# Performance work log

Measured on AMD Instinct MI355X. Metric: run time of the kernel, lower is better.

The kernel has to match this reference:

```python
import jax, jax.numpy as jnp
import numpy as np

TEMPERATURE = 0.1

def setup_inputs() -> dict:
    key = jax.random.key(0)
    k1, k2 = jax.random.split(key)
    A = jax.random.normal(k1, (16, 2048, 256), dtype=jnp.float32)
    B = jax.random.normal(k2, (16, 2048, 256), dtype=jnp.float32)
    return {"A": A, "B": B}

def _l2norm(x):
    # F.normalize(p=2, dim=-1): x / max(||x||, eps), eps=1e-12
    n = jnp.sqrt(jnp.sum(x * x, axis=-1, keepdims=True))
    return x / jnp.maximum(n, 1e-12)

def _nce_dir(sim):
    # sim: (B, N, N) logits; labels are the diagonal (row n -> col n)
    # mean over all B*N rows of (logsumexp(row) - row[label])
    lse = jax.nn.logsumexp(sim, axis=-1)            # (B, N)
    diag = jnp.diagonal(sim, axis1=-2, axis2=-1)    # (B, N)
    return jnp.mean(lse - diag)

def reference(A, B):
    emb1 = _l2norm(A)
    emb2 = _l2norm(B)
    sim12 = jnp.einsum("bnc,bmc->bnm", emb1, emb2) / TEMPERATURE  # (B, N, N)
    # sim21 is sim12 transposed per batch; reuse instead of a second bmm
    sim21 = jnp.swapaxes(sim12, -1, -2)
    return _nce_dir(sim12) + _nce_dir(sim21)
```

## Files before the change

### kernel.cpp

```cpp
#include <hip/hip_runtime.h>
#include <hip/hip_bf16.h>

typedef __attribute__((ext_vector_type(8))) __bf16 bf16x8;
typedef __attribute__((ext_vector_type(16))) float f32x16;

#define SCALE_L2E 14.4269504088896f
#define NTOT 32768

#define AS_GLOBAL __attribute__((address_space(1)))
#define AS_LDS    __attribute__((address_space(3)))

__device__ inline void async_copy16(const void* g, void* l) {
    __builtin_amdgcn_global_load_lds((const AS_GLOBAL void*)g, (AS_LDS void*)l, 16, 0, 0);
}

__device__ inline unsigned int f2bf(float f) {
    unsigned int u = __builtin_bit_cast(unsigned int, f);
    u += 0x7fffu + ((u >> 16) & 1u);
    return u >> 16;
}

__device__ inline uint4 pack8(float4 x, float4 y, float s) {
    uint4 r;
    r.x = f2bf(x.x * s) | (f2bf(x.y * s) << 16);
    r.y = f2bf(x.z * s) | (f2bf(x.w * s) << 16);
    r.z = f2bf(y.x * s) | (f2bf(y.y * s) << 16);
    r.w = f2bf(y.z * s) | (f2bf(y.w * s) << 16);
    return r;
}

__device__ inline float dot8(float4 x, float4 y) {
    return x.x*y.x + x.y*y.y + x.z*y.z + x.w*y.w;
}

__global__ __launch_bounds__(256) void nrm_kernel(
        const float* __restrict__ A, const float* __restrict__ B,
        uint4* __restrict__ E1f, uint4* __restrict__ E2f,
        float* __restrict__ diagPart, float* __restrict__ scalars,
        unsigned int* __restrict__ counter) {
    __shared__ uint4 E1lds[1024];
    __shared__ uint4 E2lds[1024];
    __shared__ float part[4];

    const int tid = threadIdx.x, w = tid >> 6, l = tid & 63;
    const int q = l & 31, h = l >> 5;
    const int wid = blockIdx.x * 4 + w;

    const float4* A4 = (const float4*)A + ((size_t)wid * 8 + h) * 64 + q * 2;
    const float4* B4 = (const float4*)B + ((size_t)wid * 8 + h) * 64 + q * 2;

    float4 a[8], bb[8];
    #pragma unroll
    for (int i = 0; i < 4; ++i) {
        a[2*i]    = A4[i * 128];
        a[2*i+1]  = A4[i * 128 + 1];
        bb[2*i]   = B4[i * 128];
        bb[2*i+1] = B4[i * 128 + 1];
    }

    float ddAcc = 0.f;
    #pragma unroll
    for (int i = 0; i < 4; ++i) {
        float sa = dot8(a[2*i], a[2*i]) + dot8(a[2*i+1], a[2*i+1]);
        float sb = dot8(bb[2*i], bb[2*i]) + dot8(bb[2*i+1], bb[2*i+1]);
        float dd = dot8(a[2*i], bb[2*i]) + dot8(a[2*i+1], bb[2*i+1]);
        #pragma unroll
        for (int off = 1; off <= 16; off <<= 1) {
            sa += __shfl_xor(sa, off);
            sb += __shfl_xor(sb, off);
            dd += __shfl_xor(dd, off);
        }
        const float ia = 1.0f / fmaxf(sqrtf(sa), 1e-12f);
        const float ib = 1.0f / fmaxf(sqrtf(sb), 1e-12f);
        if (q == 0) ddAcc += dd * ia * ib * 10.0f;

        const int row32 = w * 8 + i * 2 + h;
        const int idx   = (q >> 1) * 64 + (q & 1) * 32 + row32;
        const int idxs  = idx ^ ((idx >> 5) & 7);
        E1lds[idxs] = pack8(a[2*i], a[2*i+1], ia * SCALE_L2E);
        E2lds[idxs] = pack8(bb[2*i], bb[2*i+1], ib);
    }

    #pragma unroll
    for (int off = 1; off <= 32; off <<= 1) ddAcc += __shfl_xor(ddAcc, off);
    if (l == 0) part[w] = ddAcc;
    __syncthreads();

    {
        uint4* g1 = E1f + (size_t)blockIdx.x * 1024;
        uint4* g2 = E2f + (size_t)blockIdx.x * 1024;
        #pragma unroll
        for (int j = 0; j < 4; ++j) {
            const int t = j * 256 + tid;
            const int ts = t ^ ((t >> 5) & 7);
            g1[t] = E1lds[ts];
            g2[t] = E2lds[ts];
        }
    }

    if (tid == 0) diagPart[blockIdx.x] = part[0] + part[1] + part[2] + part[3];
    if (blockIdx.x == 0 && tid == 0) { scalars[0] = 0.f; *counter = 0u; }
}

__global__ __launch_bounds__(256, 2) void gemm_kernel(
        const bf16x8* __restrict__ E1f, const uint4* __restrict__ E2f,
        float* __restrict__ colPart, float* __restrict__ rowPart) {
    __shared__ bf16x8 Bbuf[2][2048];
    __shared__ float colLDS[2048];

    const int tid = threadIdx.x, w = tid >> 6, l = tid & 63;
    const int b = blockIdx.x & 15;
    const int ct = (blockIdx.x >> 4) & 3, rt = blockIdx.x >> 6;

    for (int i = l; i < 512; i += 64) colLDS[w * 512 + i] = 0.f;

    const uint4* Bb = E2f + (size_t)b * 65536 + (size_t)ct * 16384 + l;

    auto stage = [&](int buf, int sg) {
        const uint4* src = Bb + (size_t)sg * 2048 + (w * 8) * 64;
        #pragma unroll
        for (int j = 0; j < 8; ++j)
            async_copy16(src + j * 64, &Bbuf[buf][(w * 8 + j) * 64]);
    };

    stage(0, 0);

    const bf16x8* Af0 = E1f + (size_t)b * 65536 + (size_t)(rt * 8 + w * 2) * 1024 + l;
    const bf16x8* Af1 = Af0 + 1024;
    bf16x8 af0[16], af1[16];
    #pragma unroll
    for (int kt = 0; kt < 16; ++kt) { af0[kt] = Af0[kt * 64]; af1[kt] = Af1[kt * 64]; }

    float rowAcc0[16], rowAcc1[16];
    #pragma unroll
    for (int r = 0; r < 16; ++r) { rowAcc0[r] = 0.f; rowAcc1[r] = 0.f; }

    auto mmpair = [&](f32x16& x0, f32x16& x1, const bf16x8* Bf) {
        #pragma unroll
        for (int r = 0; r < 16; ++r) { x0[r] = 0.f; x1[r] = 0.f; }
        __builtin_amdgcn_s_setprio(1);
        #pragma unroll
        for (int kt = 0; kt < 16; ++kt) {
            bf16x8 bfrag = Bf[kt * 64];
            x0 = __builtin_amdgcn_mfma_f32_32x32x16_bf16(af0[kt], bfrag, x0, 0, 0, 0);
            x1 = __builtin_amdgcn_mfma_f32_32x32x16_bf16(af1[kt], bfrag, x1, 0, 0, 0);
        }
        __builtin_amdgcn_s_setprio(0);
    };

    auto epi = [&](const f32x16& c, float (&rAcc)[16], int slot) {
        float p = 0.f;
        #pragma unroll
        for (int r = 0; r < 16; ++r) {
            float e = __builtin_amdgcn_exp2f(c[r]);
            rAcc[r] += e;
            p += e;
        }
        p += __shfl_xor(p, 32);
        if (l < 32) colLDS[w * 512 + slot * 32 + l] += p;
    };

    f32x16 c0, c1, d0, d1;
    #pragma unroll
    for (int r = 0; r < 16; ++r) d1[r] = -__builtin_inff();

    __syncthreads();

    for (int sg = 0; sg < 8; ++sg) {
        if (sg < 7) stage((sg + 1) & 1, sg + 1);
        const bf16x8* Bf = Bbuf[sg & 1] + l;

        mmpair(c0, c1, Bf);
        epi(d1, rowAcc1, (sg * 2 - 1) & 15);
        epi(c0, rowAcc0, sg * 2);

        mmpair(d0, d1, Bf + 1024);
        epi(c1, rowAcc1, sg * 2);
        epi(d0, rowAcc0, sg * 2 + 1);

        __syncthreads();
    }
    epi(d1, rowAcc1, 15);

    #pragma unroll
    for (int r = 0; r < 16; ++r) {
        #pragma unroll
        for (int off = 1; off <= 16; off <<= 1) {
            rowAcc0[r] += __shfl_xor(rowAcc0[r], off);
            rowAcc1[r] += __shfl_xor(rowAcc1[r], off);
        }
    }
    if ((l & 31) == 0) {
        float* rs = rowPart + (size_t)(b * 4 + ct) * 2048 + rt * 256 + w * 64 + 4 * (l >> 5);
        #pragma unroll
        for (int r = 0; r < 16; ++r) {
            const int rl = (r & 3) + 8 * (r >> 2);
            rs[rl]      = rowAcc0[r];
            rs[rl + 32] = rowAcc1[r];
        }
    }

    __syncthreads();
    float* gcol = colPart + (size_t)((b * 4 + ct) * 8 + rt) * 512;
    for (int i = tid; i < 512; i += 256)
        gcol[i] = colLDS[i] + colLDS[512 + i] + colLDS[1024 + i] + colLDS[1536 + i];
}

__global__ __launch_bounds__(256) void fin_kernel(
        const float* __restrict__ colPart, const float* __restrict__ rowPart,
        const float* __restrict__ diagPart, float* __restrict__ scalars,
        unsigned int* __restrict__ counter, float* __restrict__ out) {
    const int tid = threadIdx.x;
    float s = 0.f;
    #pragma unroll
    for (int k = 0; k < 2; ++k) {
        const int g = blockIdx.x * 512 + k * 256 + tid;
        const float* cp = colPart + (size_t)(((g >> 11) * 4 + ((g >> 9) & 3)) * 8) * 512 + (g & 511);
        float cs = 0.f;
        #pragma unroll
        for (int rt = 0; rt < 8; ++rt) cs += cp[rt * 512];
        const float* rp = rowPart + (size_t)(g >> 11) * 4 * 2048 + (g & 2047);
        float rsum = rp[0] + rp[2048] + rp[4096] + rp[6144];
        s += logf(cs) + logf(rsum);
    }
    #pragma unroll
    for (int off = 1; off <= 32; off <<= 1) s += __shfl_xor(s, off);
    __shared__ float part[4];
    __shared__ unsigned int lastFlag;
    if ((tid & 63) == 0) part[tid >> 6] = s;
    __syncthreads();
    if (tid == 0) {
        atomicAdd(&scalars[0], part[0] + part[1] + part[2] + part[3]);
        __threadfence();
        lastFlag = (atomicAdd(counter, 1u) == 63u) ? 1u : 0u;
    }
    __syncthreads();
    if (lastFlag) {
        float d = diagPart[tid] + diagPart[tid + 256]
                + diagPart[tid + 512] + diagPart[tid + 768];
        #pragma unroll
        for (int off = 1; off <= 32; off <<= 1) d += __shfl_xor(d, off);
        if ((tid & 63) == 0) part[tid >> 6] = d;
        __syncthreads();
        if (tid == 0) {
            const float diag = part[0] + part[1] + part[2] + part[3];
            const float logSum = atomicAdd(&scalars[0], 0.f);
            out[0] = (logSum - 2.0f * diag) / (float)NTOT;
        }
    }
}

extern "C" void kernel_launch(void* const* d_in, const int* in_sizes, int n_in,
                              void* d_out, int out_size, void* d_ws, size_t ws_size,
                              hipStream_t stream) {
    const float* A = (const float*)d_in[0];
    const float* B = (const float*)d_in[1];

    char* w = (char*)d_ws;
    uint4* E1f = (uint4*)w;
    uint4* E2f = (uint4*)(w + (size_t)16 * 1024 * 1024);
    float* colPart = (float*)(w + (size_t)32 * 1024 * 1024);
    float* rowPart = colPart + 262144;
    float* diagPart = rowPart + 131072;
    float* scalars = diagPart + 1024;
    unsigned int* counter = (unsigned int*)(scalars + 1);

    hipLaunchKernelGGL(nrm_kernel, dim3(1024), dim3(256), 0, stream,
                       A, B, E1f, E2f, diagPart, scalars, counter);
    hipLaunchKernelGGL(gemm_kernel, dim3(512), dim3(256), 0, stream,
                       (const bf16x8*)E1f, (const uint4*)E2f, colPart, rowPart);
    hipLaunchKernelGGL(fin_kernel, dim3(64), dim3(256), 0, stream,
                       colPart, rowPart, diagPart, scalars, counter, (float*)d_out);
}
```

Measured before the change: 140.0 us.

## Fuse final log-sum reduction into GEMM kernel via last-block counters

Removes the separate finalize kernel launch. The GEMM blocks now count completions per row group and per column group with atomic counters. The last block to finish a group computes the logs and adds them to a global scalar, and a second counter picks the block that writes the final output. This saves one kernel launch and its serial tail, at the cost of extra atomics and fences in every GEMM block.

Measured after the change: 183.3 us. 30.9% more time.

```diff
diff --git a/kernel.cpp b/kernel.cpp
--- a/kernel.cpp
+++ b/kernel.cpp
@@ -12,6 +12,10 @@
 
 __device__ inline void async_copy16(const void* g, void* l) {
     __builtin_amdgcn_global_load_lds((const AS_GLOBAL void*)g, (AS_LDS void*)l, 16, 0, 0);
+}
+
+__device__ inline float aload(const float* p) {
+    return __hip_atomic_load(p, __ATOMIC_RELAXED, __HIP_MEMORY_SCOPE_AGENT);
 }
 
 __device__ inline unsigned int f2bf(float f) {
@@ -37,7 +41,7 @@
         const float* __restrict__ A, const float* __restrict__ B,
         uint4* __restrict__ E1f, uint4* __restrict__ E2f,
         float* __restrict__ diagPart, float* __restrict__ scalars,
-        unsigned int* __restrict__ counter) {
+        unsigned int* __restrict__ cnts) {
     __shared__ uint4 E1lds[1024];
     __shared__ uint4 E2lds[1024];
     __shared__ float part[4];
@@ -99,18 +103,29 @@
     }
 
     if (tid == 0) diagPart[blockIdx.x] = part[0] + part[1] + part[2] + part[3];
-    if (blockIdx.x == 0 && tid == 0) { scalars[0] = 0.f; *counter = 0u; }
+    if (blockIdx.x == 0) {
+        if (tid == 0) scalars[0] = 0.f;
+        if (tid < 193) cnts[tid] = 0u;
+    }
 }
 
 __global__ __launch_bounds__(256, 2) void gemm_kernel(
         const bf16x8* __restrict__ E1f, const uint4* __restrict__ E2f,
-        float* __restrict__ colPart, float* __restrict__ rowPart) {
+        float* __restrict__ colPart, float* __restrict__ rowPart,
+        const float* __restrict__ diagPart, float* __restrict__ scalars,
+        unsigned int* __restrict__ cnts, float* __restrict__ out) {
     __shared__ bf16x8 Bbuf[2][2048];
     __shared__ float colLDS[2048];
+    __shared__ float redbuf[4];
+    __shared__ unsigned int rrS, rcS, isLastS;
 
     const int tid = threadIdx.x, w = tid >> 6, l = tid & 63;
     const int b = blockIdx.x & 15;
     const int ct = (blockIdx.x >> 4) & 3, rt = blockIdx.x >> 6;
+
+    unsigned int* cntRow = cnts;
+    unsigned int* cntCol = cnts + 128;
+    unsigned int* cnt2   = cnts + 192;
 
     for (int i = l; i < 512; i += 64) colLDS[w * 512 + i] = 0.f;
 
@@ -204,47 +219,66 @@
     float* gcol = colPart + (size_t)((b * 4 + ct) * 8 + rt) * 512;
     for (int i = tid; i < 512; i += 256)
         gcol[i] = colLDS[i] + colLDS[512 + i] + colLDS[1024 + i] + colLDS[1536 + i];
-}
-
-__global__ __launch_bounds__(256) void fin_kernel(
-        const float* __restrict__ colPart, const float* __restrict__ rowPart,
-        const float* __restrict__ diagPart, float* __restrict__ scalars,
-        unsigned int* __restrict__ counter, float* __restrict__ out) {
-    const int tid = threadIdx.x;
-    float s = 0.f;
-    #pragma unroll
-    for (int k = 0; k < 2; ++k) {
-        const int g = blockIdx.x * 512 + k * 256 + tid;
-        const float* cp = colPart + (size_t)(((g >> 11) * 4 + ((g >> 9) & 3)) * 8) * 512 + (g & 511);
-        float cs = 0.f;
-        #pragma unroll
-        for (int rt = 0; rt < 8; ++rt) cs += cp[rt * 512];
-        const float* rp = rowPart + (size_t)(g >> 11) * 4 * 2048 + (g & 2047);
-        float rsum = rp[0] + rp[2048] + rp[4096] + rp[6144];
-        s += logf(cs) + logf(rsum);
-    }
-    #pragma unroll
-    for (int off = 1; off <= 32; off <<= 1) s += __shfl_xor(s, off);
-    __shared__ float part[4];
-    __shared__ unsigned int lastFlag;
-    if ((tid & 63) == 0) part[tid >> 6] = s;
+
+    __threadfence();
     __syncthreads();
     if (tid == 0) {
-        atomicAdd(&scalars[0], part[0] + part[1] + part[2] + part[3]);
-        __threadfence();
-        lastFlag = (atomicAdd(counter, 1u) == 63u) ? 1u : 0u;
-    }
-    __syncthreads();
-    if (lastFlag) {
+        isLastS = 0u;
+        rrS = atomicAdd(&cntRow[b * 8 + rt], 1u);
+        rcS = atomicAdd(&cntCol[b * 4 + ct], 1u);
+    }
+    __syncthreads();
+    const bool doRow = (rrS == 3u), doCol = (rcS == 7u);
+    if (doRow || doCol) __threadfence();
+
+    auto blockSum = [&](float v) {
+        #pragma unroll
+        for (int off = 1; off <= 32; off <<= 1) v += __shfl_xor(v, off);
+        if (l == 0) redbuf[w] = v;
+        __syncthreads();
+        float t = redbuf[0] + redbuf[1] + redbuf[2] + redbuf[3];
+        __syncthreads();
+        return t;
+    };
+
+    if (doRow) {
+        const float* rp = rowPart + (size_t)(b * 4) * 2048 + rt * 256 + tid;
+        float rsum = aload(rp) + aload(rp + 2048) + aload(rp + 4096) + aload(rp + 6144);
+        float t = blockSum(logf(rsum));
+        if (tid == 0) {
+            atomicAdd(scalars, t);
+            __threadfence();
+            if (atomicAdd(cnt2, 1u) == 191u) isLastS = 1u;
+        }
+    }
+    if (doCol) {
+        float s = 0.f;
+        #pragma unroll
+        for (int k = 0; k < 2; ++k) {
+            const float* cp = colPart + (size_t)((b * 4 + ct) * 8) * 512 + k * 256 + tid;
+            float cs = 0.f;
+            #pragma unroll
+            for (int r8 = 0; r8 < 8; ++r8) cs += aload(cp + r8 * 512);
+            s += logf(cs);
+        }
+        float t = blockSum(s);
+        if (tid == 0) {
+            atomicAdd(scalars, t);
+            __threadfence();
+            if (atomicAdd(cnt2, 1u) == 191u) isLastS = 1u;
+        }
+    }
+    __syncthreads();
+    if (isLastS) {
         float d = diagPart[tid] + diagPart[tid + 256]
                 + diagPart[tid + 512] + diagPart[tid + 768];
         #pragma unroll
         for (int off = 1; off <= 32; off <<= 1) d += __shfl_xor(d, off);
-        if ((tid & 63) == 0) part[tid >> 6] = d;
+        if (l == 0) redbuf[w] = d;
         __syncthreads();
         if (tid == 0) {
-            const float diag = part[0] + part[1] + part[2] + part[3];
-            const float logSum = atomicAdd(&scalars[0], 0.f);
+            const float diag = redbuf[0] + redbuf[1] + redbuf[2] + redbuf[3];
+            const float logSum = atomicAdd(scalars, 0.f);
             out[0] = (logSum - 2.0f * diag) / (float)NTOT;
         }
     }
@@ -263,12 +297,11 @@
     float* rowPart = colPart + 262144;
     float* diagPart = rowPart + 131072;
     float* scalars = diagPart + 1024;
-    unsigned int* counter = (unsigned int*)(scalars + 1);
+    unsigned int* cnts = (unsigned int*)(scalars + 1);
 
     hipLaunchKernelGGL(nrm_kernel, dim3(1024), dim3(256), 0, stream,
-                       A, B, E1f, E2f, diagPart, scalars, counter);
+                       A, B, E1f, E2f, diagPart, scalars, cnts);
     hipLaunchKernelGGL(gemm_kernel, dim3(512), dim3(256), 0, stream,
-                       (const bf16x8*)E1f, (const uint4*)E2f, colPart, rowPart);
-    hipLaunchKernelGGL(fin_kernel, dim3(64), dim3(256), 0, stream,
-                       colPart, rowPart, diagPart, scalars, counter, (float*)d_out);
-}
+                       (const bf16x8*)E1f, (const uint4*)E2f, colPart, rowPart,
+                       diagPart, scalars, cnts, (float*)d_out);
+}
```

## Switch B staging to triple-buffered half tiles with vmcnt-based waits

Applied to the files above, without the earlier changes.

Replaces the double-buffered 2048-entry B staging with a three-slot ring of 1024-entry sub-tiles. Two sub-tiles are prefetched ahead, and each step waits with a partial s_waitcnt vmcnt plus a raw barrier instead of a full __syncthreads. This is meant to keep async global-to-LDS loads in flight across MFMA work and to cut LDS use. The manual vmcnt counting is fragile: if the compiler emits other outstanding vector loads, the count may be wrong and data could be read before it arrives.

Measured after the change: 137.9 us. Within noise of the previous version (-1.5%).

```diff
diff --git a/kernel.cpp b/kernel.cpp
--- a/kernel.cpp
+++ b/kernel.cpp
@@ -105,7 +105,7 @@
 __global__ __launch_bounds__(256, 2) void gemm_kernel(
         const bf16x8* __restrict__ E1f, const uint4* __restrict__ E2f,
         float* __restrict__ colPart, float* __restrict__ rowPart) {
-    __shared__ bf16x8 Bbuf[2][2048];
+    __shared__ bf16x8 Bbuf[3][1024];
     __shared__ float colLDS[2048];
 
     const int tid = threadIdx.x, w = tid >> 6, l = tid & 63;
@@ -116,14 +116,15 @@
 
     const uint4* Bb = E2f + (size_t)b * 65536 + (size_t)ct * 16384 + l;
 
-    auto stage = [&](int buf, int sg) {
-        const uint4* src = Bb + (size_t)sg * 2048 + (w * 8) * 64;
-        #pragma unroll
-        for (int j = 0; j < 8; ++j)
-            async_copy16(src + j * 64, &Bbuf[buf][(w * 8 + j) * 64]);
+    auto stage = [&](int s) {
+        const uint4* src = Bb + (size_t)s * 1024 + (w * 4) * 64;
+        #pragma unroll
+        for (int j = 0; j < 4; ++j)
+            async_copy16(src + j * 64, &Bbuf[s % 3][(w * 4 + j) * 64]);
     };
 
-    stage(0, 0);
+    stage(0);
+    stage(1);
 
     const bf16x8* Af0 = E1f + (size_t)b * 65536 + (size_t)(rt * 8 + w * 2) * 1024 + l;
     const bf16x8* Af1 = Af0 + 1024;
@@ -164,22 +165,33 @@
     #pragma unroll
     for (int r = 0; r < 16; ++r) d1[r] = -__builtin_inff();
 
-    __syncthreads();
-
-    for (int sg = 0; sg < 8; ++sg) {
-        if (sg < 7) stage((sg + 1) & 1, sg + 1);
-        const bf16x8* Bf = Bbuf[sg & 1] + l;
-
-        mmpair(c0, c1, Bf);
-        epi(d1, rowAcc1, (sg * 2 - 1) & 15);
-        epi(c0, rowAcc0, sg * 2);
-
-        mmpair(d0, d1, Bf + 1024);
-        epi(c1, rowAcc1, sg * 2);
-        epi(d0, rowAcc0, sg * 2 + 1);
-
-        __syncthreads();
-    }
+    for (int sp = 0; sp < 7; ++sp) {
+        const int s0 = sp * 2, s1 = sp * 2 + 1;
+
+        asm volatile("s_waitcnt vmcnt(4)" ::: "memory");
+        __builtin_amdgcn_s_barrier();
+        stage(s0 + 2);
+        mmpair(c0, c1, Bbuf[s0 % 3] + l);
+        epi(d1, rowAcc1, (s0 - 1) & 15);
+        epi(c0, rowAcc0, s0);
+
+        asm volatile("s_waitcnt vmcnt(4)" ::: "memory");
+        __builtin_amdgcn_s_barrier();
+        stage(s1 + 2);
+        mmpair(d0, d1, Bbuf[s1 % 3] + l);
+        epi(c1, rowAcc1, s1 - 1);
+        epi(d0, rowAcc0, s1);
+    }
+    asm volatile("s_waitcnt vmcnt(4)" ::: "memory");
+    __builtin_amdgcn_s_barrier();
+    mmpair(c0, c1, Bbuf[14 % 3] + l);
+    epi(d1, rowAcc1, 13);
+    epi(c0, rowAcc0, 14);
+    asm volatile("s_waitcnt vmcnt(0)" ::: "memory");
+    __builtin_amdgcn_s_barrier();
+    mmpair(d0, d1, Bbuf[15 % 3] + l);
+    epi(c1, rowAcc1, 14);
+    epi(d0, rowAcc0, 15);
     epi(d1, rowAcc1, 15);
 
     #pragma unroll
```
